# Kernel optimization log

Hardware: AMD Instinct MI355X
Metric: run time of the kernel (lower is better)

The kernel has to match this reference:

```python
import jax, jax.numpy as jnp
import numpy as np

W_DIM = 512
IN_CH = 512
OUT_CH = 3
CLAMP = 256.0


def setup_inputs() -> dict:
    key = jax.random.key(0)
    k1, k2, k3, k4 = jax.random.split(key, 4)
    B, H, Wd = 32, 128, 128
    return {
        "x": jax.random.normal(k1, (B, IN_CH, H, Wd), dtype=jnp.float32),
        "w": jax.random.normal(k2, (B, W_DIM), dtype=jnp.float32),
        "affine_weight": jax.random.normal(k3, (IN_CH, W_DIM), dtype=jnp.float32),
        "affine_bias": jnp.ones((IN_CH,), dtype=jnp.float32),
        "weight": jax.random.normal(k4, (OUT_CH, IN_CH, 1, 1), dtype=jnp.float32),
        "bias": jnp.zeros((OUT_CH,), dtype=jnp.float32),
    }


def reference(x, w, affine_weight, affine_bias, weight, bias):
    # FullyConnectedLayer: out = w @ (weight / sqrt(w_dim)).T + bias
    fc_gain = np.float32(1.0 / np.sqrt(W_DIM))
    styles = w @ (affine_weight * fc_gain).T + affine_bias  # [B, in_ch]
    # ToRGB weight_gain = 1/sqrt(in_channels * k^2), k=1
    weight_gain = np.float32(1.0 / np.sqrt(IN_CH))
    styles = styles * weight_gain
    # modulated 1x1 conv, demodulate=False: fold per-sample styles into the GEMM
    wk = weight[:, :, 0, 0]  # [out_ch, in_ch]
    out = jnp.einsum('bihw,oi,bi->bohw', x, wk, styles)  # [B, out_ch, H, W]
    # fused bias + clamp (bias_act with clamp=conv_clamp)
    out = out + bias[None, :, None, None]
    return jnp.clip(out, -CLAMP, CLAMP)
```

## Files before the change

### kernel.cpp

```cpp
#include <hip/hip_runtime.h>

#define W_DIM   512
#define IN_CH   512
#define OUT_CH  3
#define HW      16384
#define BATCH   32
#define CLAMP_V 256.0f

#define GAIN 0.04419417382415922f

__global__ __launch_bounds__(256) void styles_kernel(
    const float* __restrict__ w,
    const float* __restrict__ aw,
    const float* __restrict__ ab,
    const float* __restrict__ wk,
    float* __restrict__ m)
{
    const int wid  = blockIdx.x * (blockDim.x >> 6) + (threadIdx.x >> 6);
    const int lane = threadIdx.x & 63;
    const int b = wid >> 9;
    const int i = wid & 511;

    const float* wrow = w  + b * W_DIM;
    const float* arow = aw + i * W_DIM;

    float sum = 0.0f;
    #pragma unroll
    for (int k = lane; k < W_DIM; k += 64)
        sum += wrow[k] * arow[k];

    #pragma unroll
    for (int off = 32; off > 0; off >>= 1)
        sum += __shfl_xor(sum, off, 64);

    const float style = (sum * GAIN + ab[i]) * GAIN;

    if (lane < OUT_CH)
        m[(b * OUT_CH + lane) * IN_CH + i] = wk[lane * IN_CH + i] * style;
}

__global__ __launch_bounds__(256) void torgb_kernel(
    const float* __restrict__ x,
    const float* __restrict__ m,
    const float* __restrict__ bias,
    float* __restrict__ out)
{
    __shared__ float sm[OUT_CH * IN_CH];

    const int b   = blockIdx.x >> 4;
    const int blk = blockIdx.x & 15;

    for (int t = threadIdx.x; t < OUT_CH * IN_CH; t += 256)
        sm[t] = m[b * OUT_CH * IN_CH + t];
    __syncthreads();

    const int p4 = blk * 256 + threadIdx.x;
    const float4* xb = (const float4*)(x + (size_t)b * IN_CH * HW) + p4;

    float4 a0 = {0.f, 0.f, 0.f, 0.f};
    float4 a1 = {0.f, 0.f, 0.f, 0.f};
    float4 a2 = {0.f, 0.f, 0.f, 0.f};

    #pragma unroll 8
    for (int i = 0; i < IN_CH; ++i) {
        const float4 xv = xb[i * (HW / 4)];
        const float m0 = sm[i];
        const float m1 = sm[IN_CH + i];
        const float m2 = sm[2 * IN_CH + i];
        a0.x = fmaf(xv.x, m0, a0.x); a0.y = fmaf(xv.y, m0, a0.y);
        a0.z = fmaf(xv.z, m0, a0.z); a0.w = fmaf(xv.w, m0, a0.w);
        a1.x = fmaf(xv.x, m1, a1.x); a1.y = fmaf(xv.y, m1, a1.y);
        a1.z = fmaf(xv.z, m1, a1.z); a1.w = fmaf(xv.w, m1, a1.w);
        a2.x = fmaf(xv.x, m2, a2.x); a2.y = fmaf(xv.y, m2, a2.y);
        a2.z = fmaf(xv.z, m2, a2.z); a2.w = fmaf(xv.w, m2, a2.w);
    }

    const float b0 = bias[0], b1 = bias[1], b2 = bias[2];

    auto clamp4 = [](float4 v, float bb) {
        float4 r;
        r.x = fminf(fmaxf(v.x + bb, -CLAMP_V), CLAMP_V);
        r.y = fminf(fmaxf(v.y + bb, -CLAMP_V), CLAMP_V);
        r.z = fminf(fmaxf(v.z + bb, -CLAMP_V), CLAMP_V);
        r.w = fminf(fmaxf(v.w + bb, -CLAMP_V), CLAMP_V);
        return r;
    };

    float4* ob = (float4*)(out + (size_t)b * OUT_CH * HW) + p4;
    ob[0]            = clamp4(a0, b0);
    ob[HW / 4]       = clamp4(a1, b1);
    ob[2 * (HW / 4)] = clamp4(a2, b2);
}

extern "C" void kernel_launch(void* const* d_in, const int* in_sizes, int n_in,
                              void* d_out, int out_size, void* d_ws, size_t ws_size,
                              hipStream_t stream) {
    const float* x    = (const float*)d_in[0];
    const float* w    = (const float*)d_in[1];
    const float* aw   = (const float*)d_in[2];
    const float* ab   = (const float*)d_in[3];
    const float* wk   = (const float*)d_in[4];
    const float* bias = (const float*)d_in[5];
    float* out = (float*)d_out;
    float* m   = (float*)d_ws;

    styles_kernel<<<BATCH * IN_CH / 4, 256, 0, stream>>>(w, aw, ab, wk, m);

    torgb_kernel<<<BATCH * 16, 256, 0, stream>>>(x, m, bias, out);
}
```

Before: 1.317 ms.

## Split input-channel reduction across blocks with a separate combine kernel

The channel reduction is split into 8 slices, each computed by its own block, so the grid grows from 512 to 4096 blocks. The original grid underfilled the GPU for a memory-bound stream over x. Partial sums go to workspace, and a new combine kernel adds them and applies bias and clamp. This costs extra workspace traffic (8 partial planes written and read back) plus one more kernel launch.

```diff
diff --git a/kernel.cpp b/kernel.cpp
--- a/kernel.cpp
+++ b/kernel.cpp
@@ -6,6 +6,8 @@
 #define HW      16384
 #define BATCH   32
 #define CLAMP_V 256.0f
+#define SPLIT   8
+#define CH_PER  (IN_CH / SPLIT)
 
 #define GAIN 0.04419417382415922f
 
@@ -39,34 +41,38 @@
         m[(b * OUT_CH + lane) * IN_CH + i] = wk[lane * IN_CH + i] * style;
 }
 
-__global__ __launch_bounds__(256) void torgb_kernel(
+__global__ __launch_bounds__(256, 4) void torgb_part(
     const float* __restrict__ x,
     const float* __restrict__ m,
-    const float* __restrict__ bias,
-    float* __restrict__ out)
+    float* __restrict__ part)
 {
-    __shared__ float sm[OUT_CH * IN_CH];
+    __shared__ float sm[OUT_CH * CH_PER];
 
-    const int b   = blockIdx.x >> 4;
-    const int blk = blockIdx.x & 15;
+    const int idx = blockIdx.x;
+    const int blk = idx & 15;
+    const int b   = (idx >> 4) & 31;
+    const int s   = idx >> 9;
 
-    for (int t = threadIdx.x; t < OUT_CH * IN_CH; t += 256)
-        sm[t] = m[b * OUT_CH * IN_CH + t];
+    if (threadIdx.x < OUT_CH * CH_PER) {
+        const int o = threadIdx.x / CH_PER;
+        const int i = threadIdx.x % CH_PER;
+        sm[threadIdx.x] = m[(b * OUT_CH + o) * IN_CH + s * CH_PER + i];
+    }
     __syncthreads();
 
     const int p4 = blk * 256 + threadIdx.x;
-    const float4* xb = (const float4*)(x + (size_t)b * IN_CH * HW) + p4;
+    const float4* xb = (const float4*)(x + ((size_t)b * IN_CH + s * CH_PER) * HW) + p4;
 
     float4 a0 = {0.f, 0.f, 0.f, 0.f};
     float4 a1 = {0.f, 0.f, 0.f, 0.f};
     float4 a2 = {0.f, 0.f, 0.f, 0.f};
 
     #pragma unroll 8
-    for (int i = 0; i < IN_CH; ++i) {
+    for (int i = 0; i < CH_PER; ++i) {
         const float4 xv = xb[i * (HW / 4)];
         const float m0 = sm[i];
-        const float m1 = sm[IN_CH + i];
-        const float m2 = sm[2 * IN_CH + i];
+        const float m1 = sm[CH_PER + i];
+        const float m2 = sm[2 * CH_PER + i];
         a0.x = fmaf(xv.x, m0, a0.x); a0.y = fmaf(xv.y, m0, a0.y);
         a0.z = fmaf(xv.z, m0, a0.z); a0.w = fmaf(xv.w, m0, a0.w);
         a1.x = fmaf(xv.x, m1, a1.x); a1.y = fmaf(xv.y, m1, a1.y);
@@ -75,21 +81,37 @@
         a2.z = fmaf(xv.z, m2, a2.z); a2.w = fmaf(xv.w, m2, a2.w);
     }
 
-    const float b0 = bias[0], b1 = bias[1], b2 = bias[2];
+    float4* pb = (float4*)(part + ((size_t)(s * BATCH + b) * OUT_CH) * HW) + p4;
+    pb[0]            = a0;
+    pb[HW / 4]       = a1;
+    pb[2 * (HW / 4)] = a2;
+}
 
-    auto clamp4 = [](float4 v, float bb) {
-        float4 r;
-        r.x = fminf(fmaxf(v.x + bb, -CLAMP_V), CLAMP_V);
-        r.y = fminf(fmaxf(v.y + bb, -CLAMP_V), CLAMP_V);
-        r.z = fminf(fmaxf(v.z + bb, -CLAMP_V), CLAMP_V);
-        r.w = fminf(fmaxf(v.w + bb, -CLAMP_V), CLAMP_V);
-        return r;
-    };
+__global__ __launch_bounds__(256) void combine_kernel(
+    const float* __restrict__ part,
+    const float* __restrict__ bias,
+    float* __restrict__ out)
+{
+    const int j = blockIdx.x * 256 + threadIdx.x;
+    const int PLANE4 = BATCH * OUT_CH * (HW / 4);
 
-    float4* ob = (float4*)(out + (size_t)b * OUT_CH * HW) + p4;
-    ob[0]            = clamp4(a0, b0);
-    ob[HW / 4]       = clamp4(a1, b1);
-    ob[2 * (HW / 4)] = clamp4(a2, b2);
+    const float4* p4 = (const float4*)part;
+    float4 acc = p4[j];
+    #pragma unroll
+    for (int s = 1; s < SPLIT; ++s) {
+        const float4 v = p4[s * PLANE4 + j];
+        acc.x += v.x; acc.y += v.y; acc.z += v.z; acc.w += v.w;
+    }
+
+    const int o = (j >> 12) % OUT_CH;
+    const float bb = bias[o];
+
+    float4 r;
+    r.x = fminf(fmaxf(acc.x + bb, -CLAMP_V), CLAMP_V);
+    r.y = fminf(fmaxf(acc.y + bb, -CLAMP_V), CLAMP_V);
+    r.z = fminf(fmaxf(acc.z + bb, -CLAMP_V), CLAMP_V);
+    r.w = fminf(fmaxf(acc.w + bb, -CLAMP_V), CLAMP_V);
+    ((float4*)out)[j] = r;
 }
 
 extern "C" void kernel_launch(void* const* d_in, const int* in_sizes, int n_in,
@@ -102,9 +124,11 @@
     const float* wk   = (const float*)d_in[4];
     const float* bias = (const float*)d_in[5];
     float* out = (float*)d_out;
-    float* m   = (float*)d_ws;
+
+    float* m    = (float*)d_ws;
+    float* part = m + BATCH * OUT_CH * IN_CH;
 
     styles_kernel<<<BATCH * IN_CH / 4, 256, 0, stream>>>(w, aw, ab, wk, m);
-
-    torgb_kernel<<<BATCH * 16, 256, 0, stream>>>(x, m, bias, out);
+    torgb_part<<<SPLIT * BATCH * 16, 256, 0, stream>>>(x, m, part);
+    combine_kernel<<<BATCH * OUT_CH * (HW / 4) / 256, 256, 0, stream>>>(part, bias, out);
 }
```

After: 1.347 ms. 1.02x slower.
